# Performance work log

Hardware: AMD Instinct MI355X
Metric: run time of the kernel (lower is better)

The kernel has to match this reference:

```python
import jax, jax.numpy as jnp
import numpy as np

B, N, D = 4, 4096, 256


def setup_inputs() -> dict:
    key = jax.random.key(0)
    k1, k2 = jax.random.split(key)
    val = jax.random.normal(k1, (B, N, D), dtype=jnp.float32)
    state = jax.random.normal(k2, (B, N), dtype=jnp.float32)
    return {"val": val, "state": state}


def reference(val, state):
    # pairwise_fn: scaled dot-product -> scores [B, N, N]
    scale = val.shape[-1] ** -0.5
    scores = jnp.einsum("bid,bjd->bij", val, val) * scale
    # edge_compress_fn = softsign (non-softmax compression)
    edges = scores / (1.0 + jnp.abs(scores))
    # state_weight_edges=False, val/state projections are Identity
    delta_state = jnp.einsum("bij,bj->bi", edges, state)   # [B, N]
    delta_val = jnp.einsum("bij,bjd->bid", edges, val)      # [B, N, D]
    return (delta_state, delta_val)
```

## Files before the change

### kernel.cpp

```cpp
#include <hip/hip_runtime.h>


#define B_  4
#define N_  4096
#define D_  256

typedef __attribute__((ext_vector_type(8))) short short8;
typedef __attribute__((ext_vector_type(4))) float floatx4;

__device__ __forceinline__ unsigned short f2bf(float f) {
    unsigned int u = __float_as_uint(f);
    u += 0x7fff + ((u >> 16) & 1);
    return (unsigned short)(u >> 16);
}

__device__ __forceinline__ void gl_lds16(const void* g, void* l) {
    __builtin_amdgcn_global_load_lds(
        (const __attribute__((address_space(1))) unsigned int*)g,
        (__attribute__((address_space(3))) unsigned int*)l, 16, 0, 0);
}
__device__ __forceinline__ void gl_lds4(const void* g, void* l) {
    __builtin_amdgcn_global_load_lds(
        (const __attribute__((address_space(1))) unsigned int*)g,
        (__attribute__((address_space(3))) unsigned int*)l, 4, 0, 0);
}

__global__ __launch_bounds__(256)
void prepass_kernel(const float* __restrict__ val,
                    unsigned short* __restrict__ Vb,
                    unsigned short* __restrict__ VT) {
    __shared__ unsigned short tile[64][68];
    const int t   = threadIdx.x;
    const int blk = blockIdx.x;
    const int b   = blk >> 8;
    const int it  = (blk >> 2) & 63;
    const int dt  = blk & 3;
    const int i0  = it * 64, d0 = dt * 64;
    const float*    vb  = val + (size_t)b * N_ * D_;
    unsigned short* Vbb = Vb  + (size_t)b * N_ * D_;
    unsigned short* VTb = VT  + (size_t)b * D_ * N_;

    #pragma unroll
    for (int q = 0; q < 4; ++q) {
        int idx = t + 256 * q;
        int row = idx >> 4;
        int c4  = idx & 15;
        float4 v = *(const float4*)(vb + (size_t)(i0 + row) * D_ + d0 + c4 * 4);
        ushort4 h;
        h.x = f2bf(v.x); h.y = f2bf(v.y); h.z = f2bf(v.z); h.w = f2bf(v.w);
        *(ushort4*)(Vbb + (size_t)(i0 + row) * D_ + d0 + c4 * 4) = h;
        *(ushort4*)&tile[row][c4 * 4] = h;
    }
    __syncthreads();
    #pragma unroll
    for (int q = 0; q < 4; ++q) {
        int dr = (t >> 4) + q * 16;
        int i4 = t & 15;
        ushort4 h;
        h.x = tile[i4 * 4 + 0][dr];
        h.y = tile[i4 * 4 + 1][dr];
        h.z = tile[i4 * 4 + 2][dr];
        h.w = tile[i4 * 4 + 3][dr];
        *(ushort4*)(VTb + (size_t)(d0 + dr) * N_ + i0 + i4 * 4) = h;
    }
}

__global__ __launch_bounds__(512, 2)
void prop_main(const float* __restrict__ state,
               const unsigned short* __restrict__ Vb,
               const unsigned short* __restrict__ VT,
               float* __restrict__ dvp,
               float* __restrict__ dsp_o)
{
    __shared__ __attribute__((aligned(16))) unsigned char smem[137472];

    const int t    = threadIdx.x;
    const int g    = t >> 8;
    const int w    = t >> 6;
    const int w4   = w & 3;
    const int lane = t & 63;
    const int quad = lane >> 4;
    const int l16  = lane & 15;

    const int x   = blockIdx.x;
    const int b   = x >> 6;
    const int it  = (x >> 1) & 31;
    const int jh  = x & 1;
    const int it0 = it * 128;
    const int jbase = jh * 2048;
    const int niter = 32;

    unsigned short* vjL  = (unsigned short*)(smem + 65536);
    float*          stjL = (float*)(smem + 135168);
    float*          dsredg = (float*)(smem + 135424 + g * 1024);

    const unsigned short* Vbb = Vb + (size_t)b * N_ * D_;
    const unsigned short* VTb = VT + (size_t)b * D_ * N_;
    const float*          stb = state + (size_t)b * N_;

    const int hi  = lane >> 5;
    const int p32 = lane & 31;
    const int dr8 = lane >> 3;
    const int p8  = lane & 7;

    int vgoff[4];
    int tgoff[4];
    #pragma unroll
    for (int n = 0; n < 4; ++n) {
        int r  = 2 * (w * 4 + n) + hi;
        vgoff[n] = r * 256 + (p32 ^ (r & 7)) * 8;
        int d  = 8 * (w * 4 + n) + dr8;
        tgoff[n] = d * 4096 + (p8 ^ dr8) * 8;
    }

    const int jq = w4 * 16;
    const int pA = l16 & 7;

    short8 Vi4[4][8];
    #pragma unroll
    for (int ib = 0; ib < 4; ++ib) {
        const unsigned short* ar =
            Vbb + (size_t)(it0 + g * 64 + ib * 16 + l16) * 256 + quad * 8;
        #pragma unroll
        for (int ks = 0; ks < 8; ++ks)
            Vi4[ib][ks] = *(const short8*)(ar + ks * 32);
    }

    #pragma unroll
    for (int n = 0; n < 4; ++n)
        gl_lds16(VTb + (size_t)jbase + tgoff[n], smem + (w * 4 + n) * 1024);
    #pragma unroll
    for (int n = 0; n < 4; ++n)
        gl_lds16(Vbb + (size_t)jbase * 256 + vgoff[n],
                 smem + 65536 + (w * 4 + n) * 1024);
    if (w == 0) gl_lds4(stb + jbase + lane, stjL);

    floatx4 dv[4][4];
    #pragma unroll
    for (int a = 0; a < 4; ++a)
        #pragma unroll
        for (int c = 0; c < 4; ++c)
            dv[a][c] = (floatx4){0.f, 0.f, 0.f, 0.f};
    float dsp[4] = {0.f, 0.f, 0.f, 0.f};

    for (int k = 0; k < niter; ++k) {
        const int buf = k & 1;
        unsigned short* Eshg = (unsigned short*)(smem + 98304 + g * 18432 + buf * 9216);
        unsigned short* vjtg = (unsigned short*)(smem + buf * 32768);

        __syncthreads();

        if (k + 1 < niter) {
            const size_t j0n = jbase + (size_t)(k + 1) * 64;
            #pragma unroll
            for (int n = 0; n < 4; ++n)
                gl_lds16(VTb + j0n + tgoff[n],
                         smem + (buf ^ 1) * 32768 + (w * 4 + n) * 1024);
        }

        floatx4 sa[4];
        #pragma unroll
        for (int ib = 0; ib < 4; ++ib)
            sa[ib] = (floatx4){0.f, 0.f, 0.f, 0.f};

        #pragma unroll
        for (int ks = 0; ks < 8; ++ks) {
            const int p = ((ks * 4 + quad) ^ pA) * 8;
            short8 aj = *(const short8*)&vjL[(jq + l16) * 256 + p];
            sa[0] = __builtin_amdgcn_mfma_f32_16x16x32_bf16(aj, Vi4[0][ks], sa[0], 0, 0, 0);
            sa[1] = __builtin_amdgcn_mfma_f32_16x16x32_bf16(aj, Vi4[1][ks], sa[1], 0, 0, 0);
            sa[2] = __builtin_amdgcn_mfma_f32_16x16x32_bf16(aj, Vi4[2][ks], sa[2], 0, 0, 0);
            sa[3] = __builtin_amdgcn_mfma_f32_16x16x32_bf16(aj, Vi4[3][ks], sa[3], 0, 0, 0);
        }

        float4 st4 = *(const float4*)&stjL[jq + quad * 4];
        #pragma unroll
        for (int ib = 0; ib < 4; ++ib) {
            float e0 = sa[ib][0] * __builtin_amdgcn_rcpf(16.0f + fabsf(sa[ib][0]));
            float e1 = sa[ib][1] * __builtin_amdgcn_rcpf(16.0f + fabsf(sa[ib][1]));
            float e2 = sa[ib][2] * __builtin_amdgcn_rcpf(16.0f + fabsf(sa[ib][2]));
            float e3 = sa[ib][3] * __builtin_amdgcn_rcpf(16.0f + fabsf(sa[ib][3]));
            dsp[ib] += e0 * st4.x + e1 * st4.y + e2 * st4.z + e3 * st4.w;
            uint2 pk;
            pk.x = (unsigned int)f2bf(e0) | ((unsigned int)f2bf(e1) << 16);
            pk.y = (unsigned int)f2bf(e2) | ((unsigned int)f2bf(e3) << 16);
            *(uint2*)&Eshg[(ib * 16 + l16) * 72 + jq + quad * 4] = pk;
        }
        __syncthreads();

        if (k + 1 < niter) {
            const size_t j0n = jbase + (size_t)(k + 1) * 64;
            #pragma unroll
            for (int n = 0; n < 4; ++n)
                gl_lds16(Vbb + j0n * 256 + vgoff[n],
                         smem + 65536 + (w * 4 + n) * 1024);
            if (w == 0) gl_lds4(stb + j0n + lane, stjL);
        }

        #pragma unroll
        for (int ks = 0; ks < 2; ++ks) {
            short8 af[4], bfr[4];
            #pragma unroll
            for (int a2 = 0; a2 < 4; ++a2)
                af[a2] = *(const short8*)&Eshg[(a2 * 16 + l16) * 72 + ks * 32 + quad * 8];
            #pragma unroll
            for (int c2 = 0; c2 < 4; ++c2) {
                const int d = w4 * 64 + c2 * 16 + l16;
                const int p = ((ks * 4 + quad) ^ pA) * 8;
                bfr[c2] = *(const short8*)&vjtg[d * 64 + p];
            }
            #pragma unroll
            for (int a2 = 0; a2 < 4; ++a2)
                #pragma unroll
                for (int c2 = 0; c2 < 4; ++c2)
                    dv[a2][c2] = __builtin_amdgcn_mfma_f32_16x16x32_bf16(af[a2], bfr[c2], dv[a2][c2], 0, 0, 0);
        }
    }

    float* dvo = dvp + (size_t)jh * B_ * N_ * D_ + (size_t)b * N_ * D_
                     + (size_t)(it0 + g * 64) * D_;
    #pragma unroll
    for (int a2 = 0; a2 < 4; ++a2)
        #pragma unroll
        for (int c2 = 0; c2 < 4; ++c2)
            #pragma unroll
            for (int r = 0; r < 4; ++r) {
                const int il = a2 * 16 + quad * 4 + r;
                const int d  = w4 * 64 + c2 * 16 + l16;
                dvo[(size_t)il * D_ + d] = dv[a2][c2][r];
            }

    #pragma unroll
    for (int ib = 0; ib < 4; ++ib) {
        float v = dsp[ib];
        v += __shfl_xor(v, 16);
        v += __shfl_xor(v, 32);
        dsp[ib] = v;
    }
    if (quad == 0) {
        #pragma unroll
        for (int ib = 0; ib < 4; ++ib)
            dsredg[w4 * 64 + ib * 16 + l16] = dsp[ib];
    }
    __syncthreads();
    if (t < 128) {
        const int gg = t >> 6;
        const int i  = t & 63;
        const float* dsr = (const float*)(smem + 135424 + gg * 1024);
        dsp_o[(size_t)jh * B_ * N_ + (size_t)b * N_ + it0 + gg * 64 + i]
            = dsr[i] + dsr[64 + i] + dsr[128 + i] + dsr[192 + i];
    }
}

__global__ __launch_bounds__(256)
void combine_kernel(const float4* __restrict__ dv0, const float4* __restrict__ dv1,
                    const float*  __restrict__ ds0, const float*  __restrict__ ds1,
                    float* __restrict__ out) {
    const int NDV4 = B_ * N_ * D_ / 4;
    const int NDS  = B_ * N_;
    int x = blockIdx.x * 256 + threadIdx.x;
    if (x < NDV4) {
        float4 a = dv0[x], c = dv1[x];
        float4 r;
        r.x = a.x + c.x; r.y = a.y + c.y; r.z = a.z + c.z; r.w = a.w + c.w;
        ((float4*)(out + NDS))[x] = r;
    } else {
        int y = (x - NDV4) * 4;
        if (y < NDS) {
            float4 a = *(const float4*)(ds0 + y);
            float4 c = *(const float4*)(ds1 + y);
            float4 r;
            r.x = a.x + c.x; r.y = a.y + c.y; r.z = a.z + c.z; r.w = a.w + c.w;
            *(float4*)(out + y) = r;
        }
    }
}

__global__ __launch_bounds__(256, 1)
void prop_kernel_fb(const float* __restrict__ val,
                    const float* __restrict__ state,
                    float* __restrict__ out) {
    __shared__ __attribute__((aligned(16))) unsigned short vi[64][264];
    __shared__ __attribute__((aligned(16))) unsigned short vj[64][264];
    __shared__ __attribute__((aligned(16))) unsigned short vjt[2048][8];
    __shared__ __attribute__((aligned(16))) unsigned short Esh[64][72];
    __shared__ float stj[64];
    __shared__ float dsred[2][64];

    const int t    = threadIdx.x;
    const int w    = t >> 6;
    const int lane = t & 63;
    const int quad = lane >> 4;
    const int l16  = lane & 15;
    const int b   = blockIdx.x >> 6;
    const int it0 = (blockIdx.x & 63) << 6;
    const float* valb = val   + (size_t)b * N_ * D_;
    const float* stb  = state + (size_t)b * N_;

    #pragma unroll
    for (int n = 0; n < 16; ++n) {
        int idx = t + 256 * n;
        int row = idx >> 6;
        int c4  = idx & 63;
        float4 v = *(const float4*)(valb + (size_t)(it0 + row) * D_ + c4 * 4);
        ushort4 h;
        h.x = f2bf(v.x); h.y = f2bf(v.y); h.z = f2bf(v.z); h.w = f2bf(v.w);
        *(ushort4*)&vi[row][c4 * 4] = h;
    }

    const int r0 = (w >> 1) * 32;
    const int c0 = (w & 1) * 32;
    floatx4 dv[4][4];
    #pragma unroll
    for (int a = 0; a < 4; ++a)
        #pragma unroll
        for (int c = 0; c < 4; ++c)
            dv[a][c] = (floatx4){0.f, 0.f, 0.f, 0.f};
    float dsp[8];
    #pragma unroll
    for (int k = 0; k < 8; ++k) dsp[k] = 0.f;

    for (int jt = 0; jt < 64; ++jt) {
        const int j0 = jt * 64;
        #pragma unroll
        for (int n = 0; n < 16; ++n) {
            int idx = t + 256 * n;
            int row = idx >> 6;
            int c4  = idx & 63;
            float4 v = *(const float4*)(valb + (size_t)(j0 + row) * D_ + c4 * 4);
            ushort4 h;
            h.x = f2bf(v.x); h.y = f2bf(v.y); h.z = f2bf(v.z); h.w = f2bf(v.w);
            *(ushort4*)&vj[row][c4 * 4] = h;
        }
        if (t < 64) stj[t] = stb[j0 + t];
        __syncthreads();

        #pragma unroll
        for (int n = 0; n < 8; ++n) {
            const int d  = t;
            const int jb = n;
            short8 pk;
            #pragma unroll
            for (int jj = 0; jj < 8; ++jj) pk[jj] = (short)vj[jb * 8 + jj][d];
            *(short8*)&vjt[d * 8 + (jb ^ (d & 7))][0] = pk;
        }

        floatx4 sa[2][2];
        #pragma unroll
        for (int a = 0; a < 2; ++a)
            #pragma unroll
            for (int c = 0; c < 2; ++c)
                sa[a][c] = (floatx4){0.f, 0.f, 0.f, 0.f};
        #pragma unroll
        for (int ks = 0; ks < 8; ++ks) {
            const int d0 = ks * 32 + quad * 8;
            short8 a0 = *(const short8*)&vi[r0 + l16][d0];
            short8 a1 = *(const short8*)&vi[r0 + 16 + l16][d0];
            short8 b0 = *(const short8*)&vj[c0 + l16][d0];
            short8 b1 = *(const short8*)&vj[c0 + 16 + l16][d0];
            sa[0][0] = __builtin_amdgcn_mfma_f32_16x16x32_bf16(a0, b0, sa[0][0], 0, 0, 0);
            sa[0][1] = __builtin_amdgcn_mfma_f32_16x16x32_bf16(a0, b1, sa[0][1], 0, 0, 0);
            sa[1][0] = __builtin_amdgcn_mfma_f32_16x16x32_bf16(a1, b0, sa[1][0], 0, 0, 0);
            sa[1][1] = __builtin_amdgcn_mfma_f32_16x16x32_bf16(a1, b1, sa[1][1], 0, 0, 0);
        }

        float stc0 = stj[c0 + l16];
        float stc1 = stj[c0 + 16 + l16];
        #pragma unroll
        for (int a = 0; a < 2; ++a) {
            #pragma unroll
            for (int r = 0; r < 4; ++r) {
                const int il = r0 + a * 16 + quad * 4 + r;
                float s0 = sa[a][0][r] * 0.0625f;
                float s1 = sa[a][1][r] * 0.0625f;
                float e0 = s0 / (1.0f + fabsf(s0));
                float e1 = s1 / (1.0f + fabsf(s1));
                dsp[a * 4 + r] += e0 * stc0 + e1 * stc1;
                Esh[il][c0 + l16]      = f2bf(e0);
                Esh[il][c0 + 16 + l16] = f2bf(e1);
            }
        }
        __syncthreads();

        #pragma unroll
        for (int ks = 0; ks < 2; ++ks) {
            short8 af[4], bfr[4];
            #pragma unroll
            for (int a2 = 0; a2 < 4; ++a2)
                af[a2] = *(const short8*)&Esh[a2 * 16 + l16][ks * 32 + quad * 8];
            #pragma unroll
            for (int c2 = 0; c2 < 4; ++c2) {
                const int d  = w * 64 + c2 * 16 + l16;
                const int jb = ks * 4 + quad;
                bfr[c2] = *(const short8*)&vjt[d * 8 + (jb ^ (d & 7))][0];
            }
            #pragma unroll
            for (int a2 = 0; a2 < 4; ++a2)
                #pragma unroll
                for (int c2 = 0; c2 < 4; ++c2)
                    dv[a2][c2] = __builtin_amdgcn_mfma_f32_16x16x32_bf16(af[a2], bfr[c2], dv[a2][c2], 0, 0, 0);
        }
    }

    float* dvo = out + (size_t)B_ * N_ + (size_t)b * N_ * D_;
    #pragma unroll
    for (int a2 = 0; a2 < 4; ++a2)
        #pragma unroll
        for (int c2 = 0; c2 < 4; ++c2)
            #pragma unroll
            for (int r = 0; r < 4; ++r) {
                const int i = it0 + a2 * 16 + quad * 4 + r;
                const int d = w * 64 + c2 * 16 + l16;
                dvo[(size_t)i * D_ + d] = dv[a2][c2][r];
            }

    #pragma unroll
    for (int k = 0; k < 8; ++k) {
        float v = dsp[k];
        v += __shfl_xor(v, 1);
        v += __shfl_xor(v, 2);
        v += __shfl_xor(v, 4);
        v += __shfl_xor(v, 8);
        dsp[k] = v;
    }
    if (l16 == 0) {
        #pragma unroll
        for (int a = 0; a < 2; ++a)
            #pragma unroll
            for (int r = 0; r < 4; ++r) {
                const int row = (w >> 1) * 32 + a * 16 + quad * 4 + r;
                dsred[w & 1][row] = dsp[a * 4 + r];
            }
    }
    __syncthreads();
    if (t < 64) out[(size_t)b * N_ + it0 + t] = dsred[0][t] + dsred[1][t];
}

extern "C" void kernel_launch(void* const* d_in, const int* in_sizes, int n_in,
                              void* d_out, int out_size, void* d_ws, size_t ws_size,
                              hipStream_t stream) {
    const float* val   = (const float*)d_in[0];
    const float* state = (const float*)d_in[1];
    float* out = (float*)d_out;

    const size_t nE         = (size_t)B_ * N_ * D_;
    const size_t need_base  = 2 * nE * sizeof(unsigned short);
    const size_t need_split = need_base + 2 * nE * sizeof(float)
                            + 2 * (size_t)B_ * N_ * sizeof(float);

    if (ws_size >= need_split) {
        unsigned short* Vb = (unsigned short*)d_ws;
        unsigned short* VT = Vb + nE;
        float* dvp = (float*)(VT + nE);
        float* dsp = dvp + 2 * nE;
        prepass_kernel<<<dim3(1024), dim3(256), 0, stream>>>(val, Vb, VT);
        prop_main<<<dim3(256), dim3(512), 0, stream>>>(state, Vb, VT, dvp, dsp);
        const int NDV4 = B_ * N_ * D_ / 4;
        const int NDS4 = B_ * N_ / 4;
        combine_kernel<<<dim3((NDV4 + NDS4) / 256), dim3(256), 0, stream>>>(
            (const float4*)dvp, (const float4*)(dvp + nE),
            dsp, dsp + (size_t)B_ * N_, out);
    } else {
        prop_kernel_fb<<<dim3(256), dim3(256), 0, stream>>>(val, state, out);
    }
}
```

Measured before the change: 186.2 us.

## Retile score MFMA per wave as 2x2 blocks to halve register-held row fragments

```diff
diff --git a/kernel.cpp b/kernel.cpp
--- a/kernel.cpp
+++ b/kernel.cpp
@@ -65,14 +65,14 @@
     }
 }
 
-__global__ __launch_bounds__(512, 2)
+__global__ __launch_bounds__(512, 1)
 void prop_main(const float* __restrict__ state,
                const unsigned short* __restrict__ Vb,
                const unsigned short* __restrict__ VT,
                float* __restrict__ dvp,
                float* __restrict__ dsp_o)
 {
-    __shared__ __attribute__((aligned(16))) unsigned char smem[137472];
+    __shared__ __attribute__((aligned(16))) unsigned char smem[136448];
 
     const int t    = threadIdx.x;
     const int g    = t >> 8;
@@ -92,7 +92,7 @@
 
     unsigned short* vjL  = (unsigned short*)(smem + 65536);
     float*          stjL = (float*)(smem + 135168);
-    float*          dsredg = (float*)(smem + 135424 + g * 1024);
+    float*          dsredg = (float*)(smem + 135424 + g * 512);
 
     const unsigned short* Vbb = Vb + (size_t)b * N_ * D_;
     const unsigned short* VTb = VT + (size_t)b * D_ * N_;
@@ -113,17 +113,19 @@
         tgoff[n] = d * 4096 + (p8 ^ dr8) * 8;
     }
 
-    const int jq = w4 * 16;
+    const int r0 = (w4 >> 1) * 32;
+    const int c0 = (w4 & 1) * 32;
     const int pA = l16 & 7;
 
-    short8 Vi4[4][8];
-    #pragma unroll
-    for (int ib = 0; ib < 4; ++ib) {
-        const unsigned short* ar =
-            Vbb + (size_t)(it0 + g * 64 + ib * 16 + l16) * 256 + quad * 8;
-        #pragma unroll
-        for (int ks = 0; ks < 8; ++ks)
-            Vi4[ib][ks] = *(const short8*)(ar + ks * 32);
+    short8 A0[8], A1[8];
+    {
+        const unsigned short* ar0 = Vbb + (size_t)(it0 + g * 64 + r0 + l16) * 256 + quad * 8;
+        const unsigned short* ar1 = ar0 + 16 * 256;
+        #pragma unroll
+        for (int ks = 0; ks < 8; ++ks) {
+            A0[ks] = *(const short8*)(ar0 + ks * 32);
+            A1[ks] = *(const short8*)(ar1 + ks * 32);
+        }
     }
 
     #pragma unroll
@@ -141,7 +143,7 @@
         #pragma unroll
         for (int c = 0; c < 4; ++c)
             dv[a][c] = (floatx4){0.f, 0.f, 0.f, 0.f};
-    float dsp[4] = {0.f, 0.f, 0.f, 0.f};
+    float dsp[2] = {0.f, 0.f};
 
     for (int k = 0; k < niter; ++k) {
         const int buf = k & 1;
@@ -158,33 +160,41 @@
                          smem + (buf ^ 1) * 32768 + (w * 4 + n) * 1024);
         }
 
-        floatx4 sa[4];
-        #pragma unroll
-        for (int ib = 0; ib < 4; ++ib)
-            sa[ib] = (floatx4){0.f, 0.f, 0.f, 0.f};
+        floatx4 sa[2][2];
+        #pragma unroll
+        for (int a = 0; a < 2; ++a)
+            #pragma unroll
+            for (int c = 0; c < 2; ++c)
+                sa[a][c] = (floatx4){0.f, 0.f, 0.f, 0.f};
 
         #pragma unroll
         for (int ks = 0; ks < 8; ++ks) {
             const int p = ((ks * 4 + quad) ^ pA) * 8;
-            short8 aj = *(const short8*)&vjL[(jq + l16) * 256 + p];
-            sa[0] = __builtin_amdgcn_mfma_f32_16x16x32_bf16(aj, Vi4[0][ks], sa[0], 0, 0, 0);
-            sa[1] = __builtin_amdgcn_mfma_f32_16x16x32_bf16(aj, Vi4[1][ks], sa[1], 0, 0, 0);
-            sa[2] = __builtin_amdgcn_mfma_f32_16x16x32_bf16(aj, Vi4[2][ks], sa[2], 0, 0, 0);
-            sa[3] = __builtin_amdgcn_mfma_f32_16x16x32_bf16(aj, Vi4[3][ks], sa[3], 0, 0, 0);
-        }
-
-        float4 st4 = *(const float4*)&stjL[jq + quad * 4];
-        #pragma unroll
-        for (int ib = 0; ib < 4; ++ib) {
-            float e0 = sa[ib][0] * __builtin_amdgcn_rcpf(16.0f + fabsf(sa[ib][0]));
-            float e1 = sa[ib][1] * __builtin_amdgcn_rcpf(16.0f + fabsf(sa[ib][1]));
-            float e2 = sa[ib][2] * __builtin_amdgcn_rcpf(16.0f + fabsf(sa[ib][2]));
-            float e3 = sa[ib][3] * __builtin_amdgcn_rcpf(16.0f + fabsf(sa[ib][3]));
-            dsp[ib] += e0 * st4.x + e1 * st4.y + e2 * st4.z + e3 * st4.w;
-            uint2 pk;
-            pk.x = (unsigned int)f2bf(e0) | ((unsigned int)f2bf(e1) << 16);
-            pk.y = (unsigned int)f2bf(e2) | ((unsigned int)f2bf(e3) << 16);
-            *(uint2*)&Eshg[(ib * 16 + l16) * 72 + jq + quad * 4] = pk;
+            short8 aj0 = *(const short8*)&vjL[(c0 + l16) * 256 + p];
+            short8 aj1 = *(const short8*)&vjL[(c0 + 16 + l16) * 256 + p];
+            sa[0][0] = __builtin_amdgcn_mfma_f32_16x16x32_bf16(aj0, A0[ks], sa[0][0], 0, 0, 0);
+            sa[0][1] = __builtin_amdgcn_mfma_f32_16x16x32_bf16(aj0, A1[ks], sa[0][1], 0, 0, 0);
+            sa[1][0] = __builtin_amdgcn_mfma_f32_16x16x32_bf16(aj1, A0[ks], sa[1][0], 0, 0, 0);
+            sa[1][1] = __builtin_amdgcn_mfma_f32_16x16x32_bf16(aj1, A1[ks], sa[1][1], 0, 0, 0);
+        }
+
+        float4 stq[2];
+        stq[0] = *(const float4*)&stjL[c0 + quad * 4];
+        stq[1] = *(const float4*)&stjL[c0 + 16 + quad * 4];
+        #pragma unroll
+        for (int ja = 0; ja < 2; ++ja) {
+            #pragma unroll
+            for (int ic = 0; ic < 2; ++ic) {
+                float e0 = sa[ja][ic][0] * __builtin_amdgcn_rcpf(16.0f + fabsf(sa[ja][ic][0]));
+                float e1 = sa[ja][ic][1] * __builtin_amdgcn_rcpf(16.0f + fabsf(sa[ja][ic][1]));
+                float e2 = sa[ja][ic][2] * __builtin_amdgcn_rcpf(16.0f + fabsf(sa[ja][ic][2]));
+                float e3 = sa[ja][ic][3] * __builtin_amdgcn_rcpf(16.0f + fabsf(sa[ja][ic][3]));
+                dsp[ic] += e0 * stq[ja].x + e1 * stq[ja].y + e2 * stq[ja].z + e3 * stq[ja].w;
+                uint2 pk;
+                pk.x = (unsigned int)f2bf(e0) | ((unsigned int)f2bf(e1) << 16);
+                pk.y = (unsigned int)f2bf(e2) | ((unsigned int)f2bf(e3) << 16);
+                *(uint2*)&Eshg[(r0 + ic * 16 + l16) * 72 + c0 + ja * 16 + quad * 4] = pk;
+            }
         }
         __syncthreads();
 
@@ -231,24 +241,24 @@
             }
 
     #pragma unroll
-    for (int ib = 0; ib < 4; ++ib) {
-        float v = dsp[ib];
+    for (int ic = 0; ic < 2; ++ic) {
+        float v = dsp[ic];
         v += __shfl_xor(v, 16);
         v += __shfl_xor(v, 32);
-        dsp[ib] = v;
+        dsp[ic] = v;
     }
     if (quad == 0) {
         #pragma unroll
-        for (int ib = 0; ib < 4; ++ib)
-            dsredg[w4 * 64 + ib * 16 + l16] = dsp[ib];
+        for (int ic = 0; ic < 2; ++ic)
+            dsredg[(w4 & 1) * 64 + r0 + ic * 16 + l16] = dsp[ic];
     }
     __syncthreads();
     if (t < 128) {
         const int gg = t >> 6;
         const int i  = t & 63;
-        const float* dsr = (const float*)(smem + 135424 + gg * 1024);
+        const float* dsr = (const float*)(smem + 135424 + gg * 512);
         dsp_o[(size_t)jh * B_ * N_ + (size_t)b * N_ + it0 + gg * 64 + i]
-            = dsr[i] + dsr[64 + i] + dsr[128 + i] + dsr[192 + i];
+            = dsr[i] + dsr[64 + i];
     }
 }
 
```

Result: faster. 151.5 us (-18.6%).
